# Performance work log

Hardware: AMD Instinct MI355X
Metric: run time of the kernel (lower is better)

## Reference

```python
import jax, jax.numpy as jnp
import numpy as np

B, M, N, K = 64, 1024, 1024, 128


def setup_inputs() -> dict:
    key = jax.random.key(0)
    k1, k2 = jax.random.split(key)
    # int8 operands in [-128, 127]; stored as int8 like the CUDA kernel expects
    a = jax.random.randint(k1, (B, M, K), -128, 128, dtype=jnp.int32).astype(jnp.int8)
    b = jax.random.randint(k2, (B, N, K), -128, 128, dtype=jnp.int32).astype(jnp.int8)
    # alpha = a_scale * b_scale / output_scale (scalar buffer 'a' in the module)
    alpha = jnp.float32(0.0078125)
    return {"a": a, "b": b, "alpha": alpha}


def reference(a, b, alpha):
    acc = jnp.einsum("bmk,bnk->bmn", a.astype(jnp.int32), b.astype(jnp.int32))  # [B,M,N] int32
    # fused epilogue: scale by alpha, round-to-nearest, store as int32 (s32t output)
    return jnp.round(acc.astype(jnp.float32) * alpha).astype(jnp.int32)
```

## Files before the change

### kernel.cpp

```cpp
#include <hip/hip_runtime.h>
#include <stdint.h>


typedef int v4i  __attribute__((ext_vector_type(4)));
typedef int v16i __attribute__((ext_vector_type(16)));

__device__ __forceinline__ int pack4(v4i w) {
    return (w.x & 0xFF) | ((w.y & 0xFF) << 8) | ((w.z & 0xFF) << 16) | (w.w << 24);
}

__global__ __launch_bounds__(256, 2) void bmm_s8s8_s32_kernel(
    const int*   __restrict__ A,
    const int*   __restrict__ Bm,
    const float* __restrict__ alpha_p,
    int*         __restrict__ out)
{
    __shared__ uint8_t Als[128 * 128];
    __shared__ uint8_t Bls[128 * 128];

    const int tid   = threadIdx.x;
    const int lane  = tid & 63;
    const int wave  = tid >> 6;
    const int half_ = lane >> 5;
    const int lrow  = lane & 31;

    const int bz = blockIdx.z;
    const int m0 = blockIdx.y << 7;
    const int n0 = blockIdx.x << 7;

    const size_t abase = ((size_t)bz * 1024 + (size_t)m0) * 128;
    const size_t bbase = ((size_t)bz * 1024 + (size_t)n0) * 128;

#pragma unroll
    for (int t = 0; t < 4; ++t) {
        const int G  = t * 256 + tid;
        const int m  = G >> 3;
        const int gp = G & 7;
        const size_t goff = (size_t)m * 128 + (size_t)gp * 16;

        v4i a0 = *(const v4i*)(A + abase + goff + 0);
        v4i a1 = *(const v4i*)(A + abase + goff + 4);
        v4i a2 = *(const v4i*)(A + abase + goff + 8);
        v4i a3 = *(const v4i*)(A + abase + goff + 12);
        v4i b0 = *(const v4i*)(Bm + bbase + goff + 0);
        v4i b1 = *(const v4i*)(Bm + bbase + goff + 4);
        v4i b2 = *(const v4i*)(Bm + bbase + goff + 8);
        v4i b3 = *(const v4i*)(Bm + bbase + goff + 12);

        v4i pa = { pack4(a0), pack4(a1), pack4(a2), pack4(a3) };
        v4i pb = { pack4(b0), pack4(b1), pack4(b2), pack4(b3) };

        const int loff = m * 128 + ((gp ^ (m & 7)) << 4);
        *(v4i*)(Als + loff) = pa;
        *(v4i*)(Bls + loff) = pb;
    }
    __syncthreads();

    const int wr    = wave >> 1;
    const int wc    = wave & 1;
    const int arow0 = wr * 64;
    const int brow0 = wc * 64;

    v16i acc[2][2] = {};

#pragma unroll
    for (int kk = 0; kk < 4; ++kk) {
        const int g = kk * 2 + half_;
        v4i af[2], bf[2];
#pragma unroll
        for (int mi = 0; mi < 2; ++mi) {
            const int m = arow0 + mi * 32 + lrow;
            af[mi] = *(const v4i*)(Als + m * 128 + ((g ^ (m & 7)) << 4));
        }
#pragma unroll
        for (int ni = 0; ni < 2; ++ni) {
            const int n = brow0 + ni * 32 + lrow;
            bf[ni] = *(const v4i*)(Bls + n * 128 + ((g ^ (n & 7)) << 4));
        }
#pragma unroll
        for (int mi = 0; mi < 2; ++mi)
#pragma unroll
            for (int ni = 0; ni < 2; ++ni)
                acc[mi][ni] = __builtin_amdgcn_mfma_i32_32x32x32_i8(
                    af[mi], bf[ni], acc[mi][ni], 0, 0, 0);
    }

    const float alpha = *alpha_p;
    int* outb = out + ((size_t)bz << 20);

#pragma unroll
    for (int mi = 0; mi < 2; ++mi) {
#pragma unroll
        for (int ni = 0; ni < 2; ++ni) {
            const int gcol = n0 + brow0 + ni * 32 + lrow;
#pragma unroll
            for (int r = 0; r < 16; ++r) {
                const int row  = (r & 3) + 8 * (r >> 2) + 4 * half_;
                const int grow = m0 + arow0 + mi * 32 + row;
                outb[(size_t)grow * 1024 + gcol] =
                    __float2int_rn((float)acc[mi][ni][r] * alpha);
            }
        }
    }
}

extern "C" void kernel_launch(void* const* d_in, const int* in_sizes, int n_in,
                              void* d_out, int out_size, void* d_ws, size_t ws_size,
                              hipStream_t stream) {
    const int*   A     = (const int*)d_in[0];
    const int*   Bm    = (const int*)d_in[1];
    const float* alpha = (const float*)d_in[2];
    int*         out   = (int*)d_out;

    dim3 grid(8, 8, 64);
    dim3 block(256);
    bmm_s8s8_s32_kernel<<<grid, block, 0, stream>>>(A, Bm, alpha, out);
}
```

Measured before the change: 350.0 us.

## Stage epilogue through LDS for coalesced 16-byte stores and repartition waves

The epilogue now writes the scaled int32 results into shared memory one 32-row chunk at a time, then re-reads them so each thread issues 16-byte row-contiguous global stores instead of scattered 4-byte stores. The wave layout changes so each wave owns a 32-column strip across all 128 rows, which loads one B fragment and four A fragments per k step. Launch bounds are raised to a minimum of 4 blocks per CU to increase occupancy. The cost is extra barriers and LDS traffic in the epilogue, plus possible register pressure under the tighter occupancy target.

```diff
diff --git a/kernel.cpp b/kernel.cpp
--- a/kernel.cpp
+++ b/kernel.cpp
@@ -9,14 +9,16 @@
     return (w.x & 0xFF) | ((w.y & 0xFF) << 8) | ((w.z & 0xFF) << 16) | (w.w << 24);
 }
 
-__global__ __launch_bounds__(256, 2) void bmm_s8s8_s32_kernel(
+__global__ __launch_bounds__(256, 4) void bmm_s8s8_s32_kernel(
     const int*   __restrict__ A,
     const int*   __restrict__ Bm,
     const float* __restrict__ alpha_p,
     int*         __restrict__ out)
 {
-    __shared__ uint8_t Als[128 * 128];
-    __shared__ uint8_t Bls[128 * 128];
+    __shared__ uint8_t smem[32768];
+    uint8_t* Als   = smem;
+    uint8_t* Bls   = smem + 16384;
+    int*     chunk = (int*)smem;
 
     const int tid   = threadIdx.x;
     const int lane  = tid & 63;
@@ -27,6 +29,8 @@
     const int bz = blockIdx.z;
     const int m0 = blockIdx.y << 7;
     const int n0 = blockIdx.x << 7;
+
+    const float alpha = *alpha_p;
 
     const size_t abase = ((size_t)bz * 1024 + (size_t)m0) * 128;
     const size_t bbase = ((size_t)bz * 1024 + (size_t)n0) * 128;
@@ -56,51 +60,43 @@
     }
     __syncthreads();
 
-    const int wr    = wave >> 1;
-    const int wc    = wave & 1;
-    const int arow0 = wr * 64;
-    const int brow0 = wc * 64;
-
-    v16i acc[2][2] = {};
+    v16i acc[4] = {};
 
 #pragma unroll
     for (int kk = 0; kk < 4; ++kk) {
         const int g = kk * 2 + half_;
-        v4i af[2], bf[2];
+        const int n = wave * 32 + lrow;
+        const v4i bf = *(const v4i*)(Bls + n * 128 + ((g ^ (n & 7)) << 4));
+        v4i af[4];
 #pragma unroll
-        for (int mi = 0; mi < 2; ++mi) {
-            const int m = arow0 + mi * 32 + lrow;
+        for (int mi = 0; mi < 4; ++mi) {
+            const int m = mi * 32 + lrow;
             af[mi] = *(const v4i*)(Als + m * 128 + ((g ^ (m & 7)) << 4));
         }
 #pragma unroll
-        for (int ni = 0; ni < 2; ++ni) {
-            const int n = brow0 + ni * 32 + lrow;
-            bf[ni] = *(const v4i*)(Bls + n * 128 + ((g ^ (n & 7)) << 4));
-        }
-#pragma unroll
-        for (int mi = 0; mi < 2; ++mi)
-#pragma unroll
-            for (int ni = 0; ni < 2; ++ni)
-                acc[mi][ni] = __builtin_amdgcn_mfma_i32_32x32x32_i8(
-                    af[mi], bf[ni], acc[mi][ni], 0, 0, 0);
+        for (int mi = 0; mi < 4; ++mi)
+            acc[mi] = __builtin_amdgcn_mfma_i32_32x32x32_i8(af[mi], bf, acc[mi], 0, 0, 0);
     }
+    __syncthreads();
 
-    const float alpha = *alpha_p;
-    int* outb = out + ((size_t)bz << 20);
+    int* outb = out + ((size_t)bz << 20) + n0;
 
 #pragma unroll
-    for (int mi = 0; mi < 2; ++mi) {
+    for (int j = 0; j < 4; ++j) {
 #pragma unroll
-        for (int ni = 0; ni < 2; ++ni) {
-            const int gcol = n0 + brow0 + ni * 32 + lrow;
+        for (int r = 0; r < 16; ++r) {
+            const int row_local = (r & 3) + 8 * (r >> 2) + 4 * half_;
+            chunk[row_local * 128 + wave * 32 + lrow] =
+                __float2int_rn((float)acc[j][r] * alpha);
+        }
+        __syncthreads();
 #pragma unroll
-            for (int r = 0; r < 16; ++r) {
-                const int row  = (r & 3) + 8 * (r >> 2) + 4 * half_;
-                const int grow = m0 + arow0 + mi * 32 + row;
-                outb[(size_t)grow * 1024 + gcol] =
-                    __float2int_rn((float)acc[mi][ni][r] * alpha);
-            }
+        for (int p = 0; p < 4; ++p) {
+            const int row_local = p * 8 + (tid >> 5);
+            const v4i v = *(const v4i*)((const uint8_t*)chunk + p * 4096 + tid * 16);
+            *(v4i*)(outb + (size_t)(m0 + j * 32 + row_local) * 1024 + (tid & 31) * 4) = v;
         }
+        if (j < 3) __syncthreads();
     }
 }
 
```

Result: no change. 350.7 us (+0.2%).
